# Kernel optimization log

Hardware: AMD Instinct MI355X
Metric: run time of the kernel (lower is better)

## Reference

```python
import jax, jax.numpy as jnp
import numpy as np

B, S, E, H = 4, 1024, 512, 16

def setup_inputs() -> dict:
    key = jax.random.key(0)
    ks = jax.random.split(key, 6)
    return {
        "x": jax.random.normal(ks[0], (B, S, E), dtype=jnp.float32),
        "Wq": jax.random.normal(ks[1], (E, E), dtype=jnp.float32) * (E ** -0.5),
        "Wk": jax.random.normal(ks[2], (E, E), dtype=jnp.float32) * (E ** -0.5),
        "Wv": jax.random.normal(ks[3], (E, E), dtype=jnp.float32) * (E ** -0.5),
        "W1": jax.random.normal(ks[4], (H, 2 * E), dtype=jnp.float32) * ((2 * E) ** -0.5),
        "b1": jnp.zeros((H,), dtype=jnp.float32),
        "W2": jax.random.normal(ks[5], (1, H), dtype=jnp.float32) * (H ** -0.5),
        "b2": jnp.zeros((1,), dtype=jnp.float32),
    }

def reference(x, Wq, Wk, Wv, W1, b1, W2, b2):
    embed_dim = x.shape[-1]
    # nn.Linear: y = x @ W.T
    Q = jnp.einsum('bse,oe->bso', x, Wq)
    K = jnp.einsum('bse,oe->bso', x, Wk)
    V = jnp.einsum('bse,oe->bso', x, Wv)
    scores = jnp.einsum('bqe,bke->bqk', Q, K) / jnp.sqrt(jnp.float32(embed_dim))
    # Estimator on concat([Q_i, K_j]): split W1 so we never materialize the
    # [B,S,S,2E] pair tensor; concat(q,k)@W1.T == q@W1[:, :E].T + k@W1[:, E:].T
    W1q, W1k = W1[:, :embed_dim], W1[:, embed_dim:]
    hq = jnp.einsum('bqe,he->bqh', Q, W1q)          # [B,S,H]
    hk = jnp.einsum('bke,he->bkh', K, W1k)          # [B,S,H]
    hid = jnp.tanh(hq[:, :, None, :] + hk[:, None, :, :] + b1)  # [B,S,S,H]
    est = jnp.einsum('bqkh,h->bqk', hid, W2[0]) + b2[0]
    attn = jax.nn.softmax(scores + est, axis=-1)
    return jnp.einsum('bqk,bke->bqe', attn, V)
```

## Files before the change

### kernel.cpp

```cpp
#include <hip/hip_runtime.h>
#include <hip/hip_fp16.h>


#define DEVI __device__ __forceinline__

typedef _Float16 half8 __attribute__((ext_vector_type(8)));
typedef _Float16 half4v __attribute__((ext_vector_type(4)));
typedef float f32x4 __attribute__((ext_vector_type(4)));

DEVI void gload16(const void* g, void* l) {
  __builtin_amdgcn_global_load_lds(
      (const __attribute__((address_space(1))) void*)g,
      (__attribute__((address_space(3))) void*)l, 16, 0, 0);
}

DEVI half8 cvt8(float4 a, float4 b) {
  half8 h;
  h[0] = (_Float16)a.x; h[1] = (_Float16)a.y; h[2] = (_Float16)a.z; h[3] = (_Float16)a.w;
  h[4] = (_Float16)b.x; h[5] = (_Float16)b.y; h[6] = (_Float16)b.z; h[7] = (_Float16)b.w;
  return h;
}

#define MEMBAR asm volatile("" ::: "memory")

__global__ __launch_bounds__(256) void k_qkv(
    const float* __restrict__ x, const float* __restrict__ Wq,
    const float* __restrict__ Wk, const float* __restrict__ Wv,
    _Float16* __restrict__ Qh, _Float16* __restrict__ Kh, _Float16* __restrict__ Vt)
{
  __shared__ _Float16 As[2 * 128 * 32], Bs[2 * 64 * 32];
  const int bid0 = blockIdx.x;
  const int bid = (bid0 & 7) * 96 + (bid0 >> 3);
  const int mt = bid / 24, ntg = bid - mt * 24;
  const int mat = ntg >> 3, ntl = ntg & 7;
  const float* W = (mat == 0) ? Wq : ((mat == 1) ? Wk : Wv);
  const float* Ag = x + (size_t)mt * 128 * 512;
  const float* Bg = W + (size_t)ntl * 64 * 512;

  const int tid = threadIdx.x;
  const int l = tid & 63, w = tid >> 6, wr = w >> 1, wc = w & 1;
  const int frow = l & 15, kof = (l >> 4) * 8;
  const int ar = tid >> 1, ac = (tid & 1) * 16;
  const int br = tid >> 2, bc = (tid & 3) * 8;

  f32x4 acc[4][2] = {};
  float4 fa0, fa1, fa2, fa3, fb0, fb1;

  auto loadT = [&](int kt) {
    const float4* pa = (const float4*)(Ag + (size_t)ar * 512 + kt + ac);
    fa0 = pa[0]; fa1 = pa[1]; fa2 = pa[2]; fa3 = pa[3];
    const float4* pb = (const float4*)(Bg + (size_t)br * 512 + kt + bc);
    fb0 = pb[0]; fb1 = pb[1];
  };
  auto writeT = [&](int buf) {
    *(half8*)(As + buf * 4096 + ar * 32 + ac)     = cvt8(fa0, fa1);
    *(half8*)(As + buf * 4096 + ar * 32 + ac + 8) = cvt8(fa2, fa3);
    *(half8*)(Bs + buf * 2048 + br * 32 + bc)     = cvt8(fb0, fb1);
  };
  auto compute = [&](int buf) {
    half8 aF[4], bF[2];
#pragma unroll
    for (int mf = 0; mf < 4; ++mf)
      aF[mf] = *(const half8*)(As + buf * 4096 + (wr * 64 + mf * 16 + frow) * 32 + kof);
#pragma unroll
    for (int nf = 0; nf < 2; ++nf)
      bF[nf] = *(const half8*)(Bs + buf * 2048 + (wc * 32 + nf * 16 + frow) * 32 + kof);
#pragma unroll
    for (int mf = 0; mf < 4; ++mf)
#pragma unroll
      for (int nf = 0; nf < 2; ++nf)
        acc[mf][nf] = __builtin_amdgcn_mfma_f32_16x16x32_f16(aF[mf], bF[nf], acc[mf][nf], 0, 0, 0);
  };

  loadT(0); writeT(0);
  __syncthreads();
  int cur = 0;
  for (int kt = 32; kt < 512; kt += 32) {
    loadT(kt);
    compute(cur);
    writeT(cur ^ 1);
    __syncthreads();
    cur ^= 1;
  }
  compute(cur);

  const int nc0 = ntl * 64 + wc * 32 + frow;
  const int mr0 = mt * 128 + wr * 64 + (l >> 4) * 4;
#pragma unroll
  for (int mf = 0; mf < 4; ++mf)
#pragma unroll
    for (int nf = 0; nf < 2; ++nf) {
      const int col = nc0 + nf * 16;
      if (mat == 0) {
#pragma unroll
        for (int r = 0; r < 4; ++r)
          Qh[(size_t)(mr0 + mf * 16 + r) * 512 + col] = (_Float16)acc[mf][nf][r];
      } else if (mat == 1) {
#pragma unroll
        for (int r = 0; r < 4; ++r)
          Kh[(size_t)(mr0 + mf * 16 + r) * 512 + col] = (_Float16)acc[mf][nf][r];
      } else {
        const int row0 = mr0 + mf * 16;
        const int bb = row0 >> 10, s0 = row0 & 1023;
        half4v hv;
#pragma unroll
        for (int r = 0; r < 4; ++r) hv[r] = (_Float16)acc[mf][nf][r];
        *(half4v*)(Vt + ((size_t)bb * 512 + col) * 1024 + s0) = hv;
      }
    }
}

__global__ __launch_bounds__(256) void k_scores(
    const _Float16* __restrict__ Qh, const _Float16* __restrict__ Kh,
    const float* __restrict__ W1, const float* __restrict__ b1,
    const float* __restrict__ W2,
    _Float16* __restrict__ P, float* __restrict__ partials)
{
  __shared__ _Float16 As[2 * 128 * 32], Bs[2 * 64 * 32];
  __shared__ _Float16 W1fq[16 * 512], W1fk[16 * 512];
  __shared__ float Eqs[128 * 17], Eks[64 * 17], w2s[16];
  const int kt = blockIdx.x, qt = blockIdx.y, b = blockIdx.z;
  const int tid = threadIdx.x;
  const int l = tid & 63, w = tid >> 6, wr = w >> 1, wc = w & 1;
  const int frow = l & 15, kof = (l >> 4) * 8;
  if (tid < 16) w2s[tid] = W2[tid];

#pragma unroll
  for (int c = tid; c < 1024; c += 256) {
    const int t = c >> 6, lj = c & 63;
    const int e0 = t * 32 + (lj >> 4) * 8;
    const float4* pq = (const float4*)(W1 + (lj & 15) * 1024 + e0);
    *(half8*)(W1fq + c * 8) = cvt8(pq[0], pq[1]);
    const float4* pk = (const float4*)(W1 + (lj & 15) * 1024 + 512 + e0);
    *(half8*)(W1fk + c * 8) = cvt8(pk[0], pk[1]);
  }

  const _Float16* Ag = Qh + (size_t)(b * 1024 + qt * 128) * 512;
  const _Float16* Bg = Kh + (size_t)(b * 1024 + kt * 64) * 512;
  const int srA = tid >> 2, scA = (tid & 3) * 8;

  f32x4 acc[4][2] = {};
  f32x4 hqA[4] = {};
  f32x4 hkA[2] = {};

  auto stage = [&](int buf, int k2) {
    gload16(Ag + (size_t)srA * 512 + k2 + scA,        As + buf * 4096 + tid * 8);
    gload16(Ag + (size_t)(srA + 64) * 512 + k2 + scA, As + buf * 4096 + (tid + 256) * 8);
    gload16(Bg + (size_t)srA * 512 + k2 + scA,        Bs + buf * 2048 + tid * 8);
  };
  auto compute = [&](int buf, int tstep) {
    half8 aF[4], bF[2];
#pragma unroll
    for (int mf = 0; mf < 4; ++mf)
      aF[mf] = *(const half8*)(As + buf * 4096 + (wr * 64 + mf * 16 + frow) * 32 + kof);
#pragma unroll
    for (int nf = 0; nf < 2; ++nf)
      bF[nf] = *(const half8*)(Bs + buf * 2048 + (wc * 32 + nf * 16 + frow) * 32 + kof);
    const half8 wqF = *(const half8*)(W1fq + tstep * 512 + l * 8);
    const half8 wkF = *(const half8*)(W1fk + tstep * 512 + l * 8);
#pragma unroll
    for (int mf = 0; mf < 4; ++mf)
#pragma unroll
      for (int nf = 0; nf < 2; ++nf)
        acc[mf][nf] = __builtin_amdgcn_mfma_f32_16x16x32_f16(aF[mf], bF[nf], acc[mf][nf], 0, 0, 0);
#pragma unroll
    for (int mf = 0; mf < 4; ++mf)
      hqA[mf] = __builtin_amdgcn_mfma_f32_16x16x32_f16(aF[mf], wqF, hqA[mf], 0, 0, 0);
#pragma unroll
    for (int nf = 0; nf < 2; ++nf)
      hkA[nf] = __builtin_amdgcn_mfma_f32_16x16x32_f16(wkF, bF[nf], hkA[nf], 0, 0, 0);
  };

  stage(0, 0);
  asm volatile("s_waitcnt lgkmcnt(0)" ::: "memory");

  int cur = 0;
  for (int t = 0; t < 15; ++t) {
    stage(cur ^ 1, 32 * (t + 1));
    asm volatile("s_waitcnt vmcnt(3)" ::: "memory");
    __builtin_amdgcn_s_barrier();
    MEMBAR;
    compute(cur, t);
    MEMBAR;
    __builtin_amdgcn_s_barrier();
    cur ^= 1;
  }
  asm volatile("s_waitcnt vmcnt(0)" ::: "memory");
  __builtin_amdgcn_s_barrier();
  MEMBAR;
  compute(cur, 15);

  const int lr0 = wr * 64 + (l >> 4) * 4;
  if (wc == 0) {
    const float b1v = b1[frow];
#pragma unroll
    for (int mf = 0; mf < 4; ++mf)
#pragma unroll
      for (int r = 0; r < 4; ++r)
        Eqs[(lr0 + mf * 16 + r) * 17 + frow] = __expf(2.f * (hqA[mf][r] + b1v));
  }
  if (wr == 0) {
#pragma unroll
    for (int nf = 0; nf < 2; ++nf)
#pragma unroll
      for (int r = 0; r < 4; ++r)
        Eks[(wc * 32 + nf * 16 + frow) * 17 + ((l >> 4) * 4 + r)] = __expf(2.f * hkA[nf][r]);
  }
  __syncthreads();

  const float scale = 0.044194173824159216f;
#pragma unroll
  for (int mf = 0; mf < 4; ++mf)
#pragma unroll
    for (int nf = 0; nf < 2; ++nf)
      acc[mf][nf] *= scale;

  const int lc0 = wc * 32 + frow;
  float w2sum = 0.f;
#pragma unroll
  for (int h = 0; h < 16; ++h) {
    const float w2v = w2s[h];
    const float tw2 = -2.f * w2v;
    w2sum += w2v;
    float Eb[2];
#pragma unroll
    for (int nf = 0; nf < 2; ++nf) Eb[nf] = Eks[(lc0 + nf * 16) * 17 + h];
#pragma unroll
    for (int mf = 0; mf < 4; ++mf)
#pragma unroll
      for (int r = 0; r < 4; ++r) {
        const float Ea = Eqs[(lr0 + mf * 16 + r) * 17 + h];
#pragma unroll
        for (int nf = 0; nf < 2; ++nf) {
          const float t = __builtin_fmaf(Ea, Eb[nf], 1.f);
          const float rc = __builtin_amdgcn_rcpf(t);
          acc[mf][nf][r] = __builtin_fmaf(tw2, rc, acc[mf][nf][r]);
        }
      }
  }

  const float bias = w2sum - 6.f;
#pragma unroll
  for (int mf = 0; mf < 4; ++mf)
#pragma unroll
    for (int nf = 0; nf < 2; ++nf)
#pragma unroll
      for (int r = 0; r < 4; ++r)
        acc[mf][nf][r] = __expf(acc[mf][nf][r] + bias);

  float rp[4][4];
#pragma unroll
  for (int mf = 0; mf < 4; ++mf)
#pragma unroll
    for (int r = 0; r < 4; ++r) {
      float s = acc[mf][0][r] + acc[mf][1][r];
#pragma unroll
      for (int off = 1; off < 16; off <<= 1) s += __shfl_xor(s, off);
      rp[mf][r] = s;
    }

  __syncthreads();
  float* sums = (float*)As;
  if (frow == 0) {
#pragma unroll
    for (int mf = 0; mf < 4; ++mf)
#pragma unroll
      for (int r = 0; r < 4; ++r)
        sums[wc * 128 + lr0 + mf * 16 + r] = rp[mf][r];
  }
  __syncthreads();
  if (tid < 128)
    partials[((size_t)b * 1024 + qt * 128 + tid) * 16 + kt] = sums[tid] + sums[128 + tid];

  _Float16* Pb = P + ((size_t)b << 20);
#pragma unroll
  for (int mf = 0; mf < 4; ++mf)
#pragma unroll
    for (int nf = 0; nf < 2; ++nf) {
      const int col = kt * 64 + lc0 + nf * 16;
#pragma unroll
      for (int r = 0; r < 4; ++r)
        Pb[(size_t)(qt * 128 + lr0 + mf * 16 + r) * 1024 + col] = (_Float16)acc[mf][nf][r];
    }
}

__global__ __launch_bounds__(256) void k_pv(
    const _Float16* __restrict__ P, const _Float16* __restrict__ Vt,
    const float* __restrict__ partials, float* __restrict__ out)
{
  __shared__ _Float16 As[2 * 64 * 32], Bs[2 * 64 * 32];
  __shared__ float rinv[64];
  const int nt = blockIdx.x, mt = blockIdx.y, b = blockIdx.z;
  const int tid = threadIdx.x;
  if (tid < 64) {
    const float4* pp = (const float4*)(partials + ((size_t)b * 1024 + mt * 64 + tid) * 16);
    float4 s0 = pp[0], s1 = pp[1], s2 = pp[2], s3 = pp[3];
    rinv[tid] = 1.f / (((s0.x + s0.y + s0.z + s0.w) + (s1.x + s1.y + s1.z + s1.w)) +
                       ((s2.x + s2.y + s2.z + s2.w) + (s3.x + s3.y + s3.z + s3.w)));
  }

  const int l = tid & 63, w = tid >> 6, wr = w >> 1, wc = w & 1;
  const int frow = l & 15, kof = (l >> 4) * 8;
  const int srow = tid >> 2, scol = (tid & 3) * 8;
  const _Float16* Ag = P + ((size_t)b << 20) + (size_t)mt * 64 * 1024 + (size_t)srow * 1024 + scol;
  const _Float16* Bg = Vt + ((size_t)b * 512 + nt * 64) * 1024 + (size_t)srow * 1024 + scol;

  f32x4 acc[2][2] = {};

  auto stage = [&](int buf, int kt2) {
    gload16(Ag + kt2, As + buf * 2048 + tid * 8);
    gload16(Bg + kt2, Bs + buf * 2048 + tid * 8);
  };
  auto compute = [&](int buf) {
    half8 aF[2], bF[2];
#pragma unroll
    for (int mf = 0; mf < 2; ++mf)
      aF[mf] = *(const half8*)(As + buf * 2048 + (wr * 32 + mf * 16 + frow) * 32 + kof);
#pragma unroll
    for (int nf = 0; nf < 2; ++nf)
      bF[nf] = *(const half8*)(Bs + buf * 2048 + (wc * 32 + nf * 16 + frow) * 32 + kof);
#pragma unroll
    for (int mf = 0; mf < 2; ++mf)
#pragma unroll
      for (int nf = 0; nf < 2; ++nf)
        acc[mf][nf] = __builtin_amdgcn_mfma_f32_16x16x32_f16(aF[mf], bF[nf], acc[mf][nf], 0, 0, 0);
  };

  stage(0, 0);
  asm volatile("s_waitcnt lgkmcnt(0)" ::: "memory");

  int cur = 0;
  for (int t = 0; t < 31; ++t) {
    stage(cur ^ 1, 32 * (t + 1));
    asm volatile("s_waitcnt vmcnt(2)" ::: "memory");
    __builtin_amdgcn_s_barrier();
    MEMBAR;
    compute(cur);
    MEMBAR;
    __builtin_amdgcn_s_barrier();
    cur ^= 1;
  }
  asm volatile("s_waitcnt vmcnt(0)" ::: "memory");
  __builtin_amdgcn_s_barrier();
  MEMBAR;
  compute(cur);

  const int lr0 = wr * 32 + (l >> 4) * 4, lc0 = wc * 32 + frow;
#pragma unroll
  for (int mf = 0; mf < 2; ++mf)
#pragma unroll
    for (int nf = 0; nf < 2; ++nf) {
      const int col = nt * 64 + lc0 + nf * 16;
#pragma unroll
      for (int r = 0; r < 4; ++r) {
        const int lrow = lr0 + mf * 16 + r;
        out[((size_t)(b * 1024 + mt * 64 + lrow)) * 512 + col] = acc[mf][nf][r] * rinv[lrow];
      }
    }
}

extern "C" void kernel_launch(void* const* d_in, const int* in_sizes, int n_in,
                              void* d_out, int out_size, void* d_ws, size_t ws_size,
                              hipStream_t stream)
{
  const float* x  = (const float*)d_in[0];
  const float* Wq = (const float*)d_in[1];
  const float* Wk = (const float*)d_in[2];
  const float* Wv = (const float*)d_in[3];
  const float* W1 = (const float*)d_in[4];
  const float* b1 = (const float*)d_in[5];
  const float* W2 = (const float*)d_in[6];
  float* out = (float*)d_out;

  char* ws = (char*)d_ws;
  size_t off = 0;
  auto alloc = [&](size_t bytes) { char* p = ws + off; off += (bytes + 255) & ~255ull; return p; };
  _Float16* Qh    = (_Float16*)alloc(4096ull * 512 * 2);
  _Float16* Kh    = (_Float16*)alloc(4096ull * 512 * 2);
  _Float16* Vt    = (_Float16*)alloc(4ull * 512 * 1024 * 2);
  float*  parts   = (float*)alloc(4096ull * 16 * 4);
  _Float16* P     = (_Float16*)alloc(4ull * 1024 * 1024 * 2);

  k_qkv<<<768, 256, 0, stream>>>(x, Wq, Wk, Wv, Qh, Kh, Vt);
  k_scores<<<dim3(16, 8, 4), 256, 0, stream>>>(Qh, Kh, W1, b1, W2, P, parts);
  k_pv<<<dim3(8, 16, 4), 256, 0, stream>>>(P, Vt, parts, out);
}
```

Measured before the change: 66.18 us.

## Prefetch two stages in QKV, stream W1 tiles, and deepen PV K-tile

```diff
diff --git a/kernel.cpp b/kernel.cpp
--- a/kernel.cpp
+++ b/kernel.cpp
@@ -22,6 +22,8 @@
 }
 
 #define MEMBAR asm volatile("" ::: "memory")
+#define LGKM0  asm volatile("s_waitcnt lgkmcnt(0)" ::: "memory")
+#define SBAR   __builtin_amdgcn_s_barrier()
 
 __global__ __launch_bounds__(256) void k_qkv(
     const float* __restrict__ x, const float* __restrict__ Wq,
@@ -44,18 +46,30 @@
   const int br = tid >> 2, bc = (tid & 3) * 8;
 
   f32x4 acc[4][2] = {};
-  float4 fa0, fa1, fa2, fa3, fb0, fb1;
-
-  auto loadT = [&](int kt) {
+  float4 a0, a1, a2, a3, a4, a5;
+  float4 b0, b1, b2, b3, b4, b5;
+
+  auto loadA = [&](int kt) {
     const float4* pa = (const float4*)(Ag + (size_t)ar * 512 + kt + ac);
-    fa0 = pa[0]; fa1 = pa[1]; fa2 = pa[2]; fa3 = pa[3];
+    a0 = pa[0]; a1 = pa[1]; a2 = pa[2]; a3 = pa[3];
     const float4* pb = (const float4*)(Bg + (size_t)br * 512 + kt + bc);
-    fb0 = pb[0]; fb1 = pb[1];
-  };
-  auto writeT = [&](int buf) {
-    *(half8*)(As + buf * 4096 + ar * 32 + ac)     = cvt8(fa0, fa1);
-    *(half8*)(As + buf * 4096 + ar * 32 + ac + 8) = cvt8(fa2, fa3);
-    *(half8*)(Bs + buf * 2048 + br * 32 + bc)     = cvt8(fb0, fb1);
+    a4 = pb[0]; a5 = pb[1];
+  };
+  auto loadB = [&](int kt) {
+    const float4* pa = (const float4*)(Ag + (size_t)ar * 512 + kt + ac);
+    b0 = pa[0]; b1 = pa[1]; b2 = pa[2]; b3 = pa[3];
+    const float4* pb = (const float4*)(Bg + (size_t)br * 512 + kt + bc);
+    b4 = pb[0]; b5 = pb[1];
+  };
+  auto writeA = [&](int buf) {
+    *(half8*)(As + buf * 4096 + ar * 32 + ac)     = cvt8(a0, a1);
+    *(half8*)(As + buf * 4096 + ar * 32 + ac + 8) = cvt8(a2, a3);
+    *(half8*)(Bs + buf * 2048 + br * 32 + bc)     = cvt8(a4, a5);
+  };
+  auto writeB = [&](int buf) {
+    *(half8*)(As + buf * 4096 + ar * 32 + ac)     = cvt8(b0, b1);
+    *(half8*)(As + buf * 4096 + ar * 32 + ac + 8) = cvt8(b2, b3);
+    *(half8*)(Bs + buf * 2048 + br * 32 + bc)     = cvt8(b4, b5);
   };
   auto compute = [&](int buf) {
     half8 aF[4], bF[2];
@@ -72,17 +86,23 @@
         acc[mf][nf] = __builtin_amdgcn_mfma_f32_16x16x32_f16(aF[mf], bF[nf], acc[mf][nf], 0, 0, 0);
   };
 
-  loadT(0); writeT(0);
-  __syncthreads();
-  int cur = 0;
-  for (int kt = 32; kt < 512; kt += 32) {
-    loadT(kt);
-    compute(cur);
-    writeT(cur ^ 1);
-    __syncthreads();
-    cur ^= 1;
-  }
-  compute(cur);
+  loadA(0); writeA(0);
+  loadB(32);
+  LGKM0; SBAR; MEMBAR;
+  for (int t = 0; t < 14; t += 2) {
+    compute(0);
+    loadA(32 * (t + 2));
+    writeB(1);
+    LGKM0; SBAR; MEMBAR;
+    compute(1);
+    loadB(32 * (t + 3));
+    writeA(0);
+    LGKM0; SBAR; MEMBAR;
+  }
+  compute(0);
+  writeB(1);
+  LGKM0; SBAR; MEMBAR;
+  compute(1);
 
   const int nc0 = ntl * 64 + wc * 32 + frow;
   const int mr0 = mt * 128 + wr * 64 + (l >> 4) * 4;
@@ -117,7 +137,7 @@
     _Float16* __restrict__ P, float* __restrict__ partials)
 {
   __shared__ _Float16 As[2 * 128 * 32], Bs[2 * 64 * 32];
-  __shared__ _Float16 W1fq[16 * 512], W1fk[16 * 512];
+  __shared__ float W1s[2 * 1024];
   __shared__ float Eqs[128 * 17], Eks[64 * 17], w2s[16];
   const int kt = blockIdx.x, qt = blockIdx.y, b = blockIdx.z;
   const int tid = threadIdx.x;
@@ -125,19 +145,14 @@
   const int frow = l & 15, kof = (l >> 4) * 8;
   if (tid < 16) w2s[tid] = W2[tid];
 
-#pragma unroll
-  for (int c = tid; c < 1024; c += 256) {
-    const int t = c >> 6, lj = c & 63;
-    const int e0 = t * 32 + (lj >> 4) * 8;
-    const float4* pq = (const float4*)(W1 + (lj & 15) * 1024 + e0);
-    *(half8*)(W1fq + c * 8) = cvt8(pq[0], pq[1]);
-    const float4* pk = (const float4*)(W1 + (lj & 15) * 1024 + 512 + e0);
-    *(half8*)(W1fk + c * 8) = cvt8(pk[0], pk[1]);
-  }
-
   const _Float16* Ag = Qh + (size_t)(b * 1024 + qt * 128) * 512;
   const _Float16* Bg = Kh + (size_t)(b * 1024 + kt * 64) * 512;
   const int srA = tid >> 2, scA = (tid & 3) * 8;
+
+  const int c127 = tid & 127, wl = c127 >> 1, wpart = c127 & 1;
+  const int whalf = tid >> 7;
+  const float* W1src = W1 + (size_t)(wl & 15) * 1024 + (wl >> 4) * 8 + wpart * 4 + whalf * 512;
+  const int w1dofs = whalf * 512 + wl * 8 + wpart * 4;
 
   f32x4 acc[4][2] = {};
   f32x4 hqA[4] = {};
@@ -147,8 +162,9 @@
     gload16(Ag + (size_t)srA * 512 + k2 + scA,        As + buf * 4096 + tid * 8);
     gload16(Ag + (size_t)(srA + 64) * 512 + k2 + scA, As + buf * 4096 + (tid + 256) * 8);
     gload16(Bg + (size_t)srA * 512 + k2 + scA,        Bs + buf * 2048 + tid * 8);
-  };
-  auto compute = [&](int buf, int tstep) {
+    gload16(W1src + k2,                               W1s + buf * 1024 + w1dofs);
+  };
+  auto compute = [&](int buf) {
     half8 aF[4], bF[2];
 #pragma unroll
     for (int mf = 0; mf < 4; ++mf)
@@ -156,8 +172,10 @@
 #pragma unroll
     for (int nf = 0; nf < 2; ++nf)
       bF[nf] = *(const half8*)(Bs + buf * 2048 + (wc * 32 + nf * 16 + frow) * 32 + kof);
-    const half8 wqF = *(const half8*)(W1fq + tstep * 512 + l * 8);
-    const half8 wkF = *(const half8*)(W1fk + tstep * 512 + l * 8);
+    const float4* wq4 = (const float4*)(W1s + buf * 1024 + l * 8);
+    const half8 wqF = cvt8(wq4[0], wq4[1]);
+    const float4* wk4 = (const float4*)(W1s + buf * 1024 + 512 + l * 8);
+    const half8 wkF = cvt8(wk4[0], wk4[1]);
 #pragma unroll
     for (int mf = 0; mf < 4; ++mf)
 #pragma unroll
@@ -172,23 +190,19 @@
   };
 
   stage(0, 0);
-  asm volatile("s_waitcnt lgkmcnt(0)" ::: "memory");
-
+  LGKM0;
   int cur = 0;
   for (int t = 0; t < 15; ++t) {
     stage(cur ^ 1, 32 * (t + 1));
-    asm volatile("s_waitcnt vmcnt(3)" ::: "memory");
-    __builtin_amdgcn_s_barrier();
-    MEMBAR;
-    compute(cur, t);
-    MEMBAR;
-    __builtin_amdgcn_s_barrier();
+    asm volatile("s_waitcnt vmcnt(4)" ::: "memory");
+    SBAR; MEMBAR;
+    compute(cur);
+    MEMBAR; SBAR;
     cur ^= 1;
   }
   asm volatile("s_waitcnt vmcnt(0)" ::: "memory");
-  __builtin_amdgcn_s_barrier();
-  MEMBAR;
-  compute(cur, 15);
+  SBAR; MEMBAR;
+  compute(cur);
 
   const int lr0 = wr * 64 + (l >> 4) * 4;
   if (wc == 0) {
@@ -288,7 +302,7 @@
     const _Float16* __restrict__ P, const _Float16* __restrict__ Vt,
     const float* __restrict__ partials, float* __restrict__ out)
 {
-  __shared__ _Float16 As[2 * 64 * 32], Bs[2 * 64 * 32];
+  __shared__ _Float16 As[2 * 64 * 64], Bs[2 * 64 * 64];
   __shared__ float rinv[64];
   const int nt = blockIdx.x, mt = blockIdx.y, b = blockIdx.z;
   const int tid = threadIdx.x;
@@ -301,48 +315,52 @@
 
   const int l = tid & 63, w = tid >> 6, wr = w >> 1, wc = w & 1;
   const int frow = l & 15, kof = (l >> 4) * 8;
-  const int srow = tid >> 2, scol = (tid & 3) * 8;
-  const _Float16* Ag = P + ((size_t)b << 20) + (size_t)mt * 64 * 1024 + (size_t)srow * 1024 + scol;
-  const _Float16* Bg = Vt + ((size_t)b * 512 + nt * 64) * 1024 + (size_t)srow * 1024 + scol;
+  const int srow = tid >> 3, scc = (tid & 7) * 8;
+  const _Float16* Ag = P + ((size_t)b << 20) + (size_t)(mt * 64 + srow) * 1024 + scc;
+  const _Float16* Bg = Vt + ((size_t)(b * 512 + nt * 64) + srow) * 1024 + scc;
 
   f32x4 acc[2][2] = {};
 
-  auto stage = [&](int buf, int kt2) {
-    gload16(Ag + kt2, As + buf * 2048 + tid * 8);
-    gload16(Bg + kt2, Bs + buf * 2048 + tid * 8);
+  auto stage = [&](int buf, int k2) {
+    gload16(Ag + k2,                    As + buf * 4096 + tid * 8);
+    gload16(Ag + (size_t)32 * 1024 + k2, As + buf * 4096 + (tid + 256) * 8);
+    gload16(Bg + k2,                    Bs + buf * 4096 + tid * 8);
+    gload16(Bg + (size_t)32 * 1024 + k2, Bs + buf * 4096 + (tid + 256) * 8);
   };
   auto compute = [&](int buf) {
-    half8 aF[2], bF[2];
+    half8 aF[2][2], bF[2][2];
 #pragma unroll
     for (int mf = 0; mf < 2; ++mf)
-      aF[mf] = *(const half8*)(As + buf * 2048 + (wr * 32 + mf * 16 + frow) * 32 + kof);
-#pragma unroll
-    for (int nf = 0; nf < 2; ++nf)
-      bF[nf] = *(const half8*)(Bs + buf * 2048 + (wc * 32 + nf * 16 + frow) * 32 + kof);
-#pragma unroll
-    for (int mf = 0; mf < 2; ++mf)
-#pragma unroll
-      for (int nf = 0; nf < 2; ++nf)
-        acc[mf][nf] = __builtin_amdgcn_mfma_f32_16x16x32_f16(aF[mf], bF[nf], acc[mf][nf], 0, 0, 0);
+#pragma unroll
+      for (int ks = 0; ks < 2; ++ks)
+        aF[mf][ks] = *(const half8*)(As + buf * 4096 + (wr * 32 + mf * 16 + frow) * 64 + ks * 32 + kof);
+#pragma unroll
+    for (int nf = 0; nf < 2; ++nf)
+#pragma unroll
+      for (int ks = 0; ks < 2; ++ks)
+        bF[nf][ks] = *(const half8*)(Bs + buf * 4096 + (wc * 32 + nf * 16 + frow) * 64 + ks * 32 + kof);
+#pragma unroll
+    for (int ks = 0; ks < 2; ++ks)
+#pragma unroll
+      for (int mf = 0; mf < 2; ++mf)
+#pragma unroll
+        for (int nf = 0; nf < 2; ++nf)
+          acc[mf][nf] = __builtin_amdgcn_mfma_f32_16x16x32_f16(aF[mf][ks], bF[nf][ks], acc[mf][nf], 0, 0, 0);
   };
 
   stage(0, 0);
-  asm volatile("s_waitcnt lgkmcnt(0)" ::: "memory");
-
+  LGKM0;
   int cur = 0;
-  for (int t = 0; t < 31; ++t) {
-    stage(cur ^ 1, 32 * (t + 1));
-    asm volatile("s_waitcnt vmcnt(2)" ::: "memory");
-    __builtin_amdgcn_s_barrier();
-    MEMBAR;
+  for (int t = 0; t < 15; ++t) {
+    stage(cur ^ 1, 64 * (t + 1));
+    asm volatile("s_waitcnt vmcnt(4)" ::: "memory");
+    SBAR; MEMBAR;
     compute(cur);
-    MEMBAR;
-    __builtin_amdgcn_s_barrier();
+    MEMBAR; SBAR;
     cur ^= 1;
   }
   asm volatile("s_waitcnt vmcnt(0)" ::: "memory");
-  __builtin_amdgcn_s_barrier();
-  MEMBAR;
+  SBAR; MEMBAR;
   compute(cur);
 
   const int lr0 = wr * 32 + (l >> 4) * 4, lc0 = wc * 32 + frow;
```

Result: slower. 75.57 us (+14.2%).
